# Performance work log

Measured on AMD Instinct MI355X. Metric: run time of the kernel, lower is better.

The kernel has to match this reference:

```python
import jax, jax.numpy as jnp
import numpy as np

NEG = float(-2**32 + 1)  # padding value used by the original module
N_HEADS = 4


def setup_inputs() -> dict:
    key = jax.random.key(0)
    ks = jax.random.split(key, 12)
    B, L, H = 16, 200, 256
    queries = jax.random.normal(ks[0], (B, L, H), jnp.float32)
    keys = jax.random.normal(ks[1], (B, L, H), jnp.float32)
    time_mask = jax.random.randint(ks[2], (B, L), 0, 2) == 1
    attn_mask = jnp.triu(jnp.ones((L, L), dtype=bool), k=1)  # causal: True = masked
    time_matrix_K = jax.random.normal(ks[3], (B, L, L, H), jnp.float32) * 0.1
    time_matrix_V = jax.random.normal(ks[4], (B, L, L, H), jnp.float32) * 0.1
    abs_pos_K = jax.random.normal(ks[5], (B, L, H), jnp.float32)
    abs_pos_V = jax.random.normal(ks[6], (B, L, H), jnp.float32)
    s = 1.0 / np.sqrt(H)
    Wq = jax.random.normal(ks[7], (H, H), jnp.float32) * s
    Wk = jax.random.normal(ks[8], (H, H), jnp.float32) * s
    Wv = jax.random.normal(ks[9], (H, H), jnp.float32) * s
    bq = jnp.zeros((H,), jnp.float32)
    bk = jnp.zeros((H,), jnp.float32)
    bv = jnp.zeros((H,), jnp.float32)
    return dict(queries=queries, keys=keys, time_mask=time_mask, attn_mask=attn_mask,
                time_matrix_K=time_matrix_K, time_matrix_V=time_matrix_V,
                abs_pos_K=abs_pos_K, abs_pos_V=abs_pos_V,
                Wq=Wq, bq=bq, Wk=Wk, bk=bk, Wv=Wv, bv=bv)


def reference(queries, keys, time_mask, attn_mask, time_matrix_K, time_matrix_V,
              abs_pos_K, abs_pos_V, Wq, bq, Wk, bk, Wv, bv):
    B, L, H = queries.shape
    h = N_HEADS
    d = H // h
    # linear projections
    Q = (queries @ Wq.T + bq).reshape(B, L, h, d)
    K = (keys @ Wk.T + bk).reshape(B, L, h, d)
    V = (keys @ Wv.T + bv).reshape(B, L, h, d)
    posK = abs_pos_K.reshape(B, L, h, d)
    posV = abs_pos_V.reshape(B, L, h, d)
    tmK = time_matrix_K.reshape(B, L, L, h, d)
    tmV = time_matrix_V.reshape(B, L, L, h, d)
    # attention scores: content + absolute-position bias + per-row time bias
    scores = jnp.einsum('blhd,bmhd->bhlm', Q, K)
    scores += jnp.einsum('blhd,bmhd->bhlm', Q, posK)
    scores += jnp.einsum('blmhd,blhd->bhlm', tmK, Q)
    scores = scores / jnp.sqrt(jnp.asarray(d, scores.dtype))
    # time_mask masks query rows; attn_mask is causal [L,L]
    mask = time_mask[:, None, :, None] | attn_mask[None, None, :, :]  # [B,1,L,L]
    scores = jnp.where(mask, NEG, scores)
    A = jax.nn.softmax(scores, axis=-1)  # [B,h,L,L]; dropout_rate=0 -> identity
    out = jnp.einsum('bhlm,bmhd->blhd', A, V)
    out += jnp.einsum('bhlm,bmhd->blhd', A, posV)
    out += jnp.einsum('bhlm,blmhd->blhd', A, tmV)
    return out.reshape(B, L, H)
```

## Files before the change

### kernel.cpp

```cpp
#include <hip/hip_runtime.h>
#include <math.h>

#define LQ 200
#define HDIM 256

template <int CTRL>
__device__ __forceinline__ float dpp_add_step(float x) {
    int y = __builtin_amdgcn_update_dpp(0, __float_as_int(x), CTRL, 0xF, 0xF, true);
    return x + __int_as_float(y);
}
__device__ __forceinline__ float reduce16(float x) {
    x = dpp_add_step<0xB1>(x);
    x = dpp_add_step<0x4E>(x);
    x = dpp_add_step<0x141>(x);
    x = dpp_add_step<0x140>(x);
    return x;
}

__global__ __launch_bounds__(256) void proj_kernel(
    const float* __restrict__ queries, const float* __restrict__ keys,
    const float* __restrict__ posK, const float* __restrict__ posV,
    const float* __restrict__ Wq, const float* __restrict__ bq,
    const float* __restrict__ Wk, const float* __restrict__ bk,
    const float* __restrict__ Wv, const float* __restrict__ bv,
    float* __restrict__ Qp, float* __restrict__ Ksum, float* __restrict__ Vsum)
{
    __shared__ float qrow[8][HDIM];
    __shared__ float krow[8][HDIM];
    const int t = threadIdx.x;
    const int blk = blockIdx.x;
    const size_t base = (size_t)blk * 8 * HDIM;

    #pragma unroll
    for (int i = 0; i < 2; ++i) {
        int idx = i * 1024 + t * 4;
        *(float4*)&qrow[0][idx] = *(const float4*)&queries[base + idx];
        *(float4*)&krow[0][idx] = *(const float4*)&keys[base + idx];
    }
    __syncthreads();

    float accQ[8], accK[8], accV[8];
    #pragma unroll
    for (int r = 0; r < 8; ++r) { accQ[r] = 0.f; accK[r] = 0.f; accV[r] = 0.f; }

    const float4* wqp = (const float4*)&Wq[t * HDIM];
    const float4* wkp = (const float4*)&Wk[t * HDIM];
    const float4* wvp = (const float4*)&Wv[t * HDIM];

    for (int k4 = 0; k4 < HDIM / 4; ++k4) {
        float4 wq = wqp[k4], wk = wkp[k4], wv = wvp[k4];
        #pragma unroll
        for (int r = 0; r < 8; ++r) {
            float4 qv = *(const float4*)&qrow[r][k4 * 4];
            float4 kv = *(const float4*)&krow[r][k4 * 4];
            accQ[r] += qv.x * wq.x + qv.y * wq.y + qv.z * wq.z + qv.w * wq.w;
            accK[r] += kv.x * wk.x + kv.y * wk.y + kv.z * wk.z + kv.w * wk.w;
            accV[r] += kv.x * wv.x + kv.y * wv.y + kv.z * wv.z + kv.w * wv.w;
        }
    }

    const float bqv = bq[t], bkv = bk[t], bvv = bv[t];
    #pragma unroll
    for (int r = 0; r < 8; ++r) {
        size_t row = (size_t)blk * 8 + r;
        Qp[row * HDIM + t]   = (accQ[r] + bqv) * 0.125f;
        Ksum[row * HDIM + t] = accK[r] + bkv + posK[row * HDIM + t];
        Vsum[row * HDIM + t] = accV[r] + bvv + posV[row * HDIM + t];
    }
}

__global__ __launch_bounds__(256, 4) void attn_fused(
    const float* __restrict__ Qp, const float* __restrict__ Ksum,
    const float* __restrict__ Vsum, const float* __restrict__ tmK,
    const float* __restrict__ tmV, const int* __restrict__ tmask,
    float* __restrict__ out)
{
    __shared__ float outp[4][HDIM];
    __shared__ float Ssh[4][4];

    const int t = threadIdx.x;
    const int w = t >> 6;
    const int ln = t & 63;
    const int h = ln >> 4;
    const int c = ln * 4;
    const int slot = blockIdx.x;
    const int l = (LQ - 1) - (slot >> 4);
    const int b = slot & 15;
    const int blk = b * LQ + l;

    const bool rowmask = (tmask[blk] != 0);

    const float* pTV = tmV + (size_t)blk * (LQ * HDIM) + w * HDIM + c;
    const float* pVS = Vsum + (size_t)b * (LQ * HDIM) + w * HDIM + c;

    float4 acc = {0.f, 0.f, 0.f, 0.f};

    if (rowmask) {
        #pragma unroll 8
        for (int i = 0; i < LQ / 4; ++i) {
            const float4 a0 = *(const float4*)&pTV[(size_t)i * (4 * HDIM)];
            const float4 b0 = *(const float4*)&pVS[(size_t)i * (4 * HDIM)];
            acc.x += a0.x + b0.x;
            acc.y += a0.y + b0.y;
            acc.z += a0.z + b0.z;
            acc.w += a0.w + b0.w;
        }
        *(float4*)&outp[w][c] = acc;
        __syncthreads();
        out[(size_t)blk * HDIM + t] =
            (outp[0][t] + outp[1][t] + outp[2][t] + outp[3][t]) * (1.0f / LQ);
    } else {
        const float* pTK = tmK + (size_t)blk * (LQ * HDIM) + w * HDIM + c;
        const float* pKS = Ksum + (size_t)b * (LQ * HDIM) + w * HDIM + c;
        const float4 Q4 = *(const float4*)&Qp[(size_t)blk * HDIM + c];
        const int n = (l >= w) ? ((l - w) >> 2) + 1 : 0;
        float S = 0.f;

        float4 rk1_0, rk1_1, rk1_2, rk1_3;
        float4 rk2_0, rk2_1, rk2_2, rk2_3;
        float4 rv1_0, rv1_1, rv1_2, rv1_3;
        float4 rv2_0, rv2_1, rv2_2, rv2_3;

        #define LOADSLOT(SL, I) do {                                          \
            rk1_##SL = *(const float4*)&pTK[(size_t)(I) * (4 * HDIM)];        \
            rk2_##SL = *(const float4*)&pKS[(size_t)(I) * (4 * HDIM)];        \
            rv1_##SL = *(const float4*)&pTV[(size_t)(I) * (4 * HDIM)];        \
            rv2_##SL = *(const float4*)&pVS[(size_t)(I) * (4 * HDIM)];        \
        } while (0)

        #define CONSUME(SL) do {                                              \
            float p = Q4.x * (rk1_##SL.x + rk2_##SL.x)                        \
                    + Q4.y * (rk1_##SL.y + rk2_##SL.y)                        \
                    + Q4.z * (rk1_##SL.z + rk2_##SL.z)                        \
                    + Q4.w * (rk1_##SL.w + rk2_##SL.w);                       \
            p = reduce16(p);                                                  \
            const float e = __expf(p);                                        \
            acc.x += e * (rv1_##SL.x + rv2_##SL.x);                           \
            acc.y += e * (rv1_##SL.y + rv2_##SL.y);                           \
            acc.z += e * (rv1_##SL.z + rv2_##SL.z);                           \
            acc.w += e * (rv1_##SL.w + rv2_##SL.w);                           \
            S += e;                                                           \
        } while (0)

        if (n > 0) LOADSLOT(0, 0);
        if (n > 1) LOADSLOT(1, 1);
        if (n > 2) LOADSLOT(2, 2);
        if (n > 3) LOADSLOT(3, 3);

        const int nfull = n & ~3;
        for (int ib = 0; ib < nfull; ib += 4) {
            CONSUME(0); if (ib + 4 < n) LOADSLOT(0, ib + 4);
            CONSUME(1); if (ib + 5 < n) LOADSLOT(1, ib + 5);
            CONSUME(2); if (ib + 6 < n) LOADSLOT(2, ib + 6);
            CONSUME(3); if (ib + 7 < n) LOADSLOT(3, ib + 7);
        }
        const int rem = n - nfull;
        if (rem > 0) CONSUME(0);
        if (rem > 1) CONSUME(1);
        if (rem > 2) CONSUME(2);

        #undef LOADSLOT
        #undef CONSUME

        *(float4*)&outp[w][c] = acc;
        if ((ln & 15) == 0) Ssh[w][h] = S;
        __syncthreads();

        const int hh = t >> 6;
        const float Stot = Ssh[0][hh] + Ssh[1][hh] + Ssh[2][hh] + Ssh[3][hh];
        out[(size_t)blk * HDIM + t] =
            (outp[0][t] + outp[1][t] + outp[2][t] + outp[3][t]) / Stot;
    }
}

extern "C" void kernel_launch(void* const* d_in, const int* in_sizes, int n_in,
                              void* d_out, int out_size, void* d_ws, size_t ws_size,
                              hipStream_t stream) {
    const float* queries = (const float*)d_in[0];
    const float* keys    = (const float*)d_in[1];
    const int*   tmask   = (const int*)d_in[2];
    const float* tmK  = (const float*)d_in[4];
    const float* tmV  = (const float*)d_in[5];
    const float* posK = (const float*)d_in[6];
    const float* posV = (const float*)d_in[7];
    const float* Wq = (const float*)d_in[8];
    const float* bq = (const float*)d_in[9];
    const float* Wk = (const float*)d_in[10];
    const float* bk = (const float*)d_in[11];
    const float* Wv = (const float*)d_in[12];
    const float* bv = (const float*)d_in[13];

    float* ws   = (float*)d_ws;
    float* Qp   = ws;
    float* Ksum = ws + 819200;
    float* Vsum = ws + 2 * 819200;
    float* out  = (float*)d_out;

    hipLaunchKernelGGL(proj_kernel, dim3(400), dim3(256), 0, stream,
                       queries, keys, posK, posV, Wq, bq, Wk, bk, Wv, bv,
                       Qp, Ksum, Vsum);
    hipLaunchKernelGGL(attn_fused, dim3(3200), dim3(256), 0, stream,
                       Qp, Ksum, Vsum, tmK, tmV, tmask, out);
}
```

Measured before the change: 227.6 us.

## Split attention into score pass, shared-memory softmax, and value pass

Replaces the single-pass streaming softmax, which loaded K and V together through a four-slot register pipeline, with three phases. Scores are first computed and written to shared memory, then a per-head softmax normalises them across the wavefront, and a second loop streams the value rows weighted by the normalised probabilities. Phase one only loads K-side data and phase two only V-side data, which cuts live registers, and the occupancy hint in launch_bounds is dropped. The cost is two extra block barriers and giving up the manual load prefetch that overlapped the K and V streams.

```diff
diff --git a/kernel.cpp b/kernel.cpp
--- a/kernel.cpp
+++ b/kernel.cpp
@@ -69,14 +69,14 @@
     }
 }
 
-__global__ __launch_bounds__(256, 4) void attn_fused(
+__global__ __launch_bounds__(256) void attn_fused(
     const float* __restrict__ Qp, const float* __restrict__ Ksum,
     const float* __restrict__ Vsum, const float* __restrict__ tmK,
     const float* __restrict__ tmV, const int* __restrict__ tmask,
     float* __restrict__ out)
 {
+    __shared__ float sc[4][204];
     __shared__ float outp[4][HDIM];
-    __shared__ float Ssh[4][4];
 
     const int t = threadIdx.x;
     const int w = t >> 6;
@@ -109,68 +109,62 @@
         __syncthreads();
         out[(size_t)blk * HDIM + t] =
             (outp[0][t] + outp[1][t] + outp[2][t] + outp[3][t]) * (1.0f / LQ);
-    } else {
-        const float* pTK = tmK + (size_t)blk * (LQ * HDIM) + w * HDIM + c;
-        const float* pKS = Ksum + (size_t)b * (LQ * HDIM) + w * HDIM + c;
-        const float4 Q4 = *(const float4*)&Qp[(size_t)blk * HDIM + c];
-        const int n = (l >= w) ? ((l - w) >> 2) + 1 : 0;
-        float S = 0.f;
+        return;
+    }
 
-        float4 rk1_0, rk1_1, rk1_2, rk1_3;
-        float4 rk2_0, rk2_1, rk2_2, rk2_3;
-        float4 rv1_0, rv1_1, rv1_2, rv1_3;
-        float4 rv2_0, rv2_1, rv2_2, rv2_3;
+    const float* pTK = tmK + (size_t)blk * (LQ * HDIM) + w * HDIM + c;
+    const float* pKS = Ksum + (size_t)b * (LQ * HDIM) + w * HDIM + c;
+    const float4 Q4 = *(const float4*)&Qp[(size_t)blk * HDIM + c];
+    const int n = (l >= w) ? ((l - w) >> 2) + 1 : 0;
 
-        #define LOADSLOT(SL, I) do {                                          \
-            rk1_##SL = *(const float4*)&pTK[(size_t)(I) * (4 * HDIM)];        \
-            rk2_##SL = *(const float4*)&pKS[(size_t)(I) * (4 * HDIM)];        \
-            rv1_##SL = *(const float4*)&pTV[(size_t)(I) * (4 * HDIM)];        \
-            rv2_##SL = *(const float4*)&pVS[(size_t)(I) * (4 * HDIM)];        \
-        } while (0)
+    #pragma unroll 2
+    for (int i = 0; i < n; ++i) {
+        const float4 k1 = *(const float4*)&pTK[(size_t)i * (4 * HDIM)];
+        const float4 k2 = *(const float4*)&pKS[(size_t)i * (4 * HDIM)];
+        float p = Q4.x * (k1.x + k2.x) + Q4.y * (k1.y + k2.y)
+                + Q4.z * (k1.z + k2.z) + Q4.w * (k1.w + k2.w);
+        p = reduce16(p);
+        if ((ln & 15) == 0) sc[h][w + 4 * i] = p;
+    }
+    __syncthreads();
 
-        #define CONSUME(SL) do {                                              \
-            float p = Q4.x * (rk1_##SL.x + rk2_##SL.x)                        \
-                    + Q4.y * (rk1_##SL.y + rk2_##SL.y)                        \
-                    + Q4.z * (rk1_##SL.z + rk2_##SL.z)                        \
-                    + Q4.w * (rk1_##SL.w + rk2_##SL.w);                       \
-            p = reduce16(p);                                                  \
-            const float e = __expf(p);                                        \
-            acc.x += e * (rv1_##SL.x + rv2_##SL.x);                           \
-            acc.y += e * (rv1_##SL.y + rv2_##SL.y);                           \
-            acc.z += e * (rv1_##SL.z + rv2_##SL.z);                           \
-            acc.w += e * (rv1_##SL.w + rv2_##SL.w);                           \
-            S += e;                                                           \
-        } while (0)
+    {
+        float e[4];
+        float sum = 0.f;
+        #pragma unroll
+        for (int j = 0; j < 4; ++j) {
+            const int m = ln + 64 * j;
+            float ev = 0.f;
+            if (m <= l) ev = __expf(sc[w][m]);
+            e[j] = ev;
+            sum += ev;
+        }
+        #pragma unroll
+        for (int msk = 1; msk < 64; msk <<= 1) sum += __shfl_xor(sum, msk);
+        const float inv = 1.0f / sum;
+        #pragma unroll
+        for (int j = 0; j < 4; ++j) {
+            const int m = ln + 64 * j;
+            if (m <= l) sc[w][m] = e[j] * inv;
+        }
+    }
+    __syncthreads();
 
-        if (n > 0) LOADSLOT(0, 0);
-        if (n > 1) LOADSLOT(1, 1);
-        if (n > 2) LOADSLOT(2, 2);
-        if (n > 3) LOADSLOT(3, 3);
+    #pragma unroll 4
+    for (int i = 0; i < n; ++i) {
+        const float a = sc[h][w + 4 * i];
+        const float4 v1 = *(const float4*)&pTV[(size_t)i * (4 * HDIM)];
+        const float4 v2 = *(const float4*)&pVS[(size_t)i * (4 * HDIM)];
+        acc.x += a * (v1.x + v2.x);
+        acc.y += a * (v1.y + v2.y);
+        acc.z += a * (v1.z + v2.z);
+        acc.w += a * (v1.w + v2.w);
+    }
 
-        const int nfull = n & ~3;
-        for (int ib = 0; ib < nfull; ib += 4) {
-            CONSUME(0); if (ib + 4 < n) LOADSLOT(0, ib + 4);
-            CONSUME(1); if (ib + 5 < n) LOADSLOT(1, ib + 5);
-            CONSUME(2); if (ib + 6 < n) LOADSLOT(2, ib + 6);
-            CONSUME(3); if (ib + 7 < n) LOADSLOT(3, ib + 7);
-        }
-        const int rem = n - nfull;
-        if (rem > 0) CONSUME(0);
-        if (rem > 1) CONSUME(1);
-        if (rem > 2) CONSUME(2);
-
-        #undef LOADSLOT
-        #undef CONSUME
-
-        *(float4*)&outp[w][c] = acc;
-        if ((ln & 15) == 0) Ssh[w][h] = S;
-        __syncthreads();
-
-        const int hh = t >> 6;
-        const float Stot = Ssh[0][hh] + Ssh[1][hh] + Ssh[2][hh] + Ssh[3][hh];
-        out[(size_t)blk * HDIM + t] =
-            (outp[0][t] + outp[1][t] + outp[2][t] + outp[3][t]) / Stot;
-    }
+    *(float4*)&outp[w][c] = acc;
+    __syncthreads();
+    out[(size_t)blk * HDIM + t] =
+        outp[0][t] + outp[1][t] + outp[2][t] + outp[3][t];
 }
 
 extern "C" void kernel_launch(void* const* d_in, const int* in_sizes, int n_in,
```

After: 229.9 us. Within noise of the previous version (+1.0%).
